# Performance work log

Hardware: AMD Instinct MI355X
Metric: run time of the kernel (lower is better)

## Reference

```python
import jax, jax.numpy as jnp
import numpy as np

NUM_GROUPS = 32
EPS = 1e-6


def group_norm(x, gamma, beta):
    # x: (B, C, H, W)
    B, C, H, W = x.shape
    g = x.reshape(B, NUM_GROUPS, C // NUM_GROUPS, H, W)
    mean = g.mean(axis=(2, 3, 4), keepdims=True)
    var = g.var(axis=(2, 3, 4), keepdims=True)
    g = (g - mean) / jnp.sqrt(var + EPS)
    g = g.reshape(B, C, H, W)
    return g * gamma[None, :, None, None] + beta[None, :, None, None]


def nin(x, W, b):
    # 1x1 linear projection over channel dim
    return jnp.einsum('bchw,cd->bdhw', x, W) + b[None, :, None, None]


def setup_inputs() -> dict:
    key = jax.random.key(0)
    ks = jax.random.split(key, 8)
    B, C, H, W = 32, 512, 32, 32
    lim = np.sqrt(3 * 0.1 / C)  # NIN init_scale=0.1 uniform limit
    return {
        'x': jax.random.normal(ks[0], (B, C, H, W), jnp.float32),
        'gamma': jnp.ones((C,), jnp.float32),
        'beta': jnp.zeros((C,), jnp.float32),
        'Wq': jax.random.uniform(ks[1], (C, C), jnp.float32, -lim, lim),
        'bq': jnp.zeros((C,), jnp.float32),
        'Wk': jax.random.uniform(ks[2], (C, C), jnp.float32, -lim, lim),
        'bk': jnp.zeros((C,), jnp.float32),
        'Wv': jax.random.uniform(ks[3], (C, C), jnp.float32, -lim, lim),
        'bv': jnp.zeros((C,), jnp.float32),
        'Wp': jax.random.normal(ks[4], (C, C), jnp.float32) * 1e-5,  # init_scale=0.0 -> ~0
        'bp': jnp.zeros((C,), jnp.float32),
    }


def reference(x, gamma, beta, Wq, bq, Wk, bk, Wv, bv, Wp, bp):
    B, C, H, W = x.shape
    h = group_norm(x, gamma, beta)
    q = nin(h, Wq, bq)
    k = nin(h, Wk, bk)
    v = nin(h, Wv, bv)
    # full (HW)x(HW) attention weights, as the original materializes
    w = jnp.einsum('bchw,bcHW->bhwHW', q, k) * (C ** -0.5)
    w = w.reshape(B, H, W, H * W)
    w = jax.nn.softmax(w, axis=-1)
    w = w.reshape(B, H, W, H, W)
    h_out = jnp.einsum('bhwHW,bcHW->bchw', w, v)
    h_out = nin(h_out, Wp, bp)
    return x + h_out
```

## Files before the change

kernel.cpp:

```cpp
#include <hip/hip_runtime.h>
#include <hip/hip_bf16.h>
#include <math.h>

typedef __attribute__((ext_vector_type(8))) short bf16x8;
typedef __attribute__((ext_vector_type(4))) float f32x4;

typedef const __attribute__((address_space(1))) unsigned int guint;
typedef __attribute__((address_space(3))) unsigned int luint;

static __device__ __forceinline__ short f2bf(float f) {
    union { float f; unsigned u; } a; a.f = f;
    unsigned r = 0x7FFFu + ((a.u >> 16) & 1u);
    return (short)((a.u + r) >> 16);
}
static __device__ __forceinline__ float bf2f(short s) {
    union { unsigned u; float f; } a;
    a.u = ((unsigned)(unsigned short)s) << 16;
    return a.f;
}

__global__ __launch_bounds__(256)
void transpose_w(const float* __restrict__ w0, const float* __restrict__ w1,
                 const float* __restrict__ w2, const float* __restrict__ w3,
                 short* __restrict__ outT, float qscale)
{
    __shared__ float ld[32][33];
    const float* W = (blockIdx.z == 0) ? w0 : (blockIdx.z == 1) ? w1
                   : (blockIdx.z == 2) ? w2 : w3;
    const float sc = (blockIdx.z == 0) ? qscale : 1.f;
    short* O = outT + (long long)blockIdx.z * 512 * 512;
    const int tx = threadIdx.x & 31, ty = threadIdx.x >> 5;
    const int c0 = blockIdx.y * 32, d0 = blockIdx.x * 32;
#pragma unroll
    for (int r = 0; r < 4; ++r)
        ld[ty + 8 * r][tx] = W[(long long)(c0 + ty + 8 * r) * 512 + d0 + tx];
    __syncthreads();
#pragma unroll
    for (int r = 0; r < 4; ++r)
        O[(long long)(d0 + ty + 8 * r) * 512 + c0 + tx] = f2bf(ld[tx][ty + 8 * r] * sc);
}

__global__ __launch_bounds__(256)
void concat_bias(const float* __restrict__ bq, const float* __restrict__ bk,
                 float* __restrict__ bqk, float qscale)
{
    int i = blockIdx.x * 256 + threadIdx.x;
    bqk[i] = (i < 512) ? bq[i] * qscale : bk[i - 512];
}

__global__ __launch_bounds__(256)
void gn_stats(const float* __restrict__ x, float2* __restrict__ stats)
{
    const int bg = blockIdx.x;
    const float4* p = reinterpret_cast<const float4*>(x + (long long)bg * 16384);
    float s = 0.f, ss = 0.f;
    for (int i = threadIdx.x; i < 4096; i += 256) {
        float4 v = p[i];
        s  += v.x + v.y + v.z + v.w;
        ss += v.x * v.x + v.y * v.y + v.z * v.z + v.w * v.w;
    }
    __shared__ float rs[256], rss[256];
    rs[threadIdx.x] = s; rss[threadIdx.x] = ss;
    __syncthreads();
    for (int o = 128; o > 0; o >>= 1) {
        if (threadIdx.x < o) { rs[threadIdx.x] += rs[threadIdx.x + o];
                               rss[threadIdx.x] += rss[threadIdx.x + o]; }
        __syncthreads();
    }
    if (threadIdx.x == 0) {
        float mean = rs[0] * (1.f / 16384.f);
        float var  = rss[0] * (1.f / 16384.f) - mean * mean;
        stats[bg] = make_float2(mean, rsqrtf(var + 1e-6f));
    }
}

__global__ __launch_bounds__(256)
void gn_apply_t(const float* __restrict__ x, const float2* __restrict__ stats,
                const float* __restrict__ gamma, const float* __restrict__ beta,
                short* __restrict__ hn)
{
    __shared__ short lds[32 * 520];
    const int t = threadIdx.x;
    const int s0 = blockIdx.x * 32;
    const int b  = blockIdx.y;
#pragma unroll
    for (int i = 0; i < 16; ++i) {
        int qi = t + 256 * i;
        int c = qi >> 3, sc = qi & 7;
        float4 v = *reinterpret_cast<const float4*>(
            x + ((long long)(b * 512 + c)) * 1024 + s0 + sc * 4);
        float2 st = stats[b * 32 + (c >> 4)];
        float ga = gamma[c], be = beta[c];
        float m = st.x, r = st.y;
        lds[(sc * 4 + 0) * 520 + c] = f2bf((v.x - m) * r * ga + be);
        lds[(sc * 4 + 1) * 520 + c] = f2bf((v.y - m) * r * ga + be);
        lds[(sc * 4 + 2) * 520 + c] = f2bf((v.z - m) * r * ga + be);
        lds[(sc * 4 + 3) * 520 + c] = f2bf((v.w - m) * r * ga + be);
    }
    __syncthreads();
#pragma unroll
    for (int i = 0; i < 8; ++i) {
        int p = t + 256 * i;
        int s = p >> 6, j = p & 63;
        float4 v = *reinterpret_cast<const float4*>(&lds[s * 520 + j * 8]);
        *reinterpret_cast<float4*>(
            hn + ((long long)(b * 1024 + s0 + s)) * 512 + j * 8) = v;
    }
}

template<int BIAS_M, int BIAS_N, int RESID, int EXPOUT, int DIVROW>
__global__ __launch_bounds__(512, 2)
void nt_gemm(const short* __restrict__ A, const short* __restrict__ B,
             void* __restrict__ Cv,
             const float* __restrict__ biasM, const float* __restrict__ biasN,
             const float* __restrict__ resid, const float* __restrict__ rs,
             int rsM, float scale, int K, int lda, int ldb, int ldc,
             long long sA, long long sB, long long sC,
             int tilesM, int tilesPerBatch)
{
    __shared__ short lsA[2][256 * 64];
    __shared__ short lsB[2][256 * 64];

    const int id = blockIdx.x;
    const int chunk = gridDim.x >> 3;
    const int gid = (id & 7) * chunk + (id >> 3);
    const int bz = gid / tilesPerBatch;
    const int tt = gid - bz * tilesPerBatch;
    const int m0 = (tt % tilesM) * 256;
    const int n0 = (tt / tilesM) * 256;

    const int t = threadIdx.x;
    const int lane = t & 63;
    const int w = t >> 6;
    const int wm = w >> 2, wn = w & 3;
    const int lr16 = lane & 15, lkg = lane >> 4;
    const int sw = lr16 & 7;

    const int srow = t >> 3;
    const int scol = ((t & 7) ^ ((t >> 3) & 7)) * 8;
    const short* gA = A + (long long)bz * sA + (long long)(m0 + srow) * lda + scol;
    const short* gB = B + (long long)bz * sB + (long long)(n0 + srow) * ldb + scol;

    f32x4 acc[8][4];
#pragma unroll
    for (int i = 0; i < 8; ++i)
#pragma unroll
        for (int j = 0; j < 4; ++j) acc[i][j] = (f32x4){0.f, 0.f, 0.f, 0.f};

    const int nk = K >> 6;

#define STAGE(buf, kt)                                                         \
    {                                                                          \
        const short* ga_ = gA + (kt) * 64;                                     \
        const short* gb_ = gB + (kt) * 64;                                     \
        _Pragma("unroll")                                                      \
        for (int c = 0; c < 4; ++c) {                                          \
            __builtin_amdgcn_global_load_lds(                                  \
                (guint*)(ga_ + (long long)(64 * c) * lda),                     \
                (luint*)&lsA[buf][t * 8 + 4096 * c], 16, 0, 0);                \
            __builtin_amdgcn_global_load_lds(                                  \
                (guint*)(gb_ + (long long)(64 * c) * ldb),                     \
                (luint*)&lsB[buf][t * 8 + 4096 * c], 16, 0, 0);                \
        }                                                                      \
    }

#define COMPUTE(buf)                                                           \
    {                                                                          \
        _Pragma("unroll")                                                      \
        for (int ks = 0; ks < 2; ++ks) {                                       \
            bf16x8 bq[4];                                                      \
            _Pragma("unroll")                                                  \
            for (int ni = 0; ni < 4; ++ni)                                     \
                bq[ni] = *reinterpret_cast<const bf16x8*>(                     \
                    &lsB[buf][(wn * 64 + ni * 16 + lr16) * 64 +                \
                              (((ks * 4 + lkg) ^ sw) * 8)]);                   \
            _Pragma("unroll")                                                  \
            for (int mq = 0; mq < 4; ++mq) {                                   \
                bf16x8 aq[2];                                                  \
                _Pragma("unroll")                                              \
                for (int z = 0; z < 2; ++z)                                    \
                    aq[z] = *reinterpret_cast<const bf16x8*>(                  \
                        &lsA[buf][(wm * 128 + (mq * 2 + z) * 16 + lr16) * 64 + \
                                  (((ks * 4 + lkg) ^ sw) * 8)]);               \
                __builtin_amdgcn_s_setprio(1);                                 \
                _Pragma("unroll")                                              \
                for (int z = 0; z < 2; ++z)                                    \
                    _Pragma("unroll")                                          \
                    for (int ni = 0; ni < 4; ++ni)                             \
                        acc[mq * 2 + z][ni] =                                  \
                            __builtin_amdgcn_mfma_f32_16x16x32_bf16(           \
                                aq[z], bq[ni], acc[mq * 2 + z][ni], 0, 0, 0);  \
                __builtin_amdgcn_s_setprio(0);                                 \
            }                                                                  \
        }                                                                      \
    }

    STAGE(0, 0);
    int cur = 0;
    for (int kt = 0; kt < nk - 1; ++kt) {
        STAGE(cur ^ 1, kt + 1);
        asm volatile("s_waitcnt vmcnt(8)" ::: "memory");
        __builtin_amdgcn_sched_barrier(0);
        __builtin_amdgcn_s_barrier();
        __builtin_amdgcn_sched_barrier(0);
        COMPUTE(cur);
        __builtin_amdgcn_sched_barrier(0);
        __builtin_amdgcn_s_barrier();
        __builtin_amdgcn_sched_barrier(0);
        cur ^= 1;
    }
    asm volatile("s_waitcnt vmcnt(0)" ::: "memory");
    __builtin_amdgcn_sched_barrier(0);
    __builtin_amdgcn_s_barrier();
    __builtin_amdgcn_sched_barrier(0);
    COMPUTE(cur);
#undef STAGE
#undef COMPUTE

#pragma unroll
    for (int mi = 0; mi < 8; ++mi) {
        float addm[4], mul[4];
#pragma unroll
        for (int j = 0; j < 4; ++j) {
            const int rrow = m0 + wm * 128 + mi * 16 + lkg * 4 + j;
            addm[j] = BIAS_M ? biasM[rrow] : 0.f;
            mul[j]  = DIVROW ? 1.f / rs[(long long)bz * rsM + rrow] : 1.f;
        }
#pragma unroll
        for (int ni = 0; ni < 4; ++ni) {
            const int col = n0 + wn * 64 + ni * 16 + lr16;
            float bn = BIAS_N ? biasN[col] : 0.f;
#pragma unroll
            for (int j = 0; j < 4; ++j) {
                const int rrow = m0 + wm * 128 + mi * 16 + lkg * 4 + j;
                float v2 = acc[mi][ni][j] + addm[j] + bn;
                v2 *= scale;
                if (EXPOUT) v2 = __expf(v2 - 8.f);
                if (DIVROW) v2 *= mul[j];
                const long long idx = (long long)rrow * ldc + col;
                if (RESID) {
                    float* Cf = (float*)Cv + (long long)bz * sC;
                    Cf[idx] = v2 + resid[(long long)bz * sC + idx];
                } else {
                    short* Cs = (short*)Cv + (long long)bz * sC;
                    Cs[idx] = f2bf(v2);
                }
            }
        }
    }
}

__global__ __launch_bounds__(256)
void rowsum_rows(const short* __restrict__ S, float* __restrict__ rs)
{
    const int wave = threadIdx.x >> 6, lane = threadIdx.x & 63;
    const long long row = (long long)blockIdx.x * 4 + wave;
    const short* p = S + row * 1024;
    bf16x8 h0 = *reinterpret_cast<const bf16x8*>(p + lane * 8);
    bf16x8 h1 = *reinterpret_cast<const bf16x8*>(p + 512 + lane * 8);
    float s = 0.f;
#pragma unroll
    for (int j = 0; j < 8; ++j) s += bf2f(h0[j]) + bf2f(h1[j]);
#pragma unroll
    for (int o = 32; o > 0; o >>= 1) s += __shfl_xor(s, o);
    if (lane == 0) rs[row] = s;
}

extern "C" void kernel_launch(void* const* d_in, const int* in_sizes, int n_in,
                              void* d_out, int out_size, void* d_ws, size_t ws_size,
                              hipStream_t stream)
{
    (void)in_sizes; (void)n_in; (void)out_size; (void)ws_size;
    const float* x     = (const float*)d_in[0];
    const float* gamma = (const float*)d_in[1];
    const float* beta  = (const float*)d_in[2];
    const float* Wq = (const float*)d_in[3];
    const float* bq = (const float*)d_in[4];
    const float* Wk = (const float*)d_in[5];
    const float* bk = (const float*)d_in[6];
    const float* Wv = (const float*)d_in[7];
    const float* bv = (const float*)d_in[8];
    const float* Wp = (const float*)d_in[9];
    const float* bp = (const float*)d_in[10];
    float* out = (float*)d_out;

    char* ws = (char*)d_ws;
    short*  expS = (short*)ws;
    short*  hn   = (short*)ws;
    short*  qkb  = (short*)(ws + (64LL << 20));
    short*  vbuf = (short*)(ws + (128LL << 20));
    short*  wT   = (short*)(ws + (160LL << 20));
    float2* stats = (float2*)(ws + (162LL << 20));
    float*  bqk   = (float*)(ws + (162LL << 20) + (16 << 10));
    float*  rs    = (float*)(ws + (162LL << 20) + (32 << 10));
    short*  ho    = qkb;

    const short* WqkT = wT;
    const short* WvT  = wT + 2 * 512 * 512;
    const short* WpT  = wT + 3 * 512 * 512;

    const float qscale = 0.044194173824159216f;

    transpose_w<<<dim3(16, 16, 4), 256, 0, stream>>>(Wq, Wk, Wv, Wp, wT, qscale);
    concat_bias<<<dim3(4), 256, 0, stream>>>(bq, bk, bqk, qscale);
    gn_stats<<<dim3(1024), 256, 0, stream>>>(x, stats);
    gn_apply_t<<<dim3(32, 32), 256, 0, stream>>>(x, stats, gamma, beta, hn);

    nt_gemm<0, 1, 0, 0, 0><<<512, 512, 0, stream>>>(
        hn, WqkT, qkb, nullptr, bqk, nullptr, nullptr, 0, 1.f,
        512, 512, 512, 1024, 1024 * 512, 0, 1024LL * 1024, 4, 16);
    nt_gemm<1, 0, 0, 0, 0><<<256, 512, 0, stream>>>(
        WvT, hn, vbuf, bv, nullptr, nullptr, nullptr, 0, 1.f,
        512, 512, 512, 1024, 0, 1024 * 512, 512 * 1024, 2, 8);
    nt_gemm<0, 0, 0, 1, 0><<<512, 512, 0, stream>>>(
        qkb, qkb + 512, expS, nullptr, nullptr, nullptr, nullptr, 0, 1.f,
        512, 1024, 1024, 1024, 1024LL * 1024, 1024LL * 1024, 1024LL * 1024, 4, 16);
    rowsum_rows<<<dim3(8192), 256, 0, stream>>>(expS, rs);
    nt_gemm<0, 0, 0, 0, 1><<<256, 512, 0, stream>>>(
        expS, vbuf, ho, nullptr, nullptr, nullptr, rs, 1024, 1.f,
        1024, 1024, 1024, 512, 1024LL * 1024, 512 * 1024, 1024 * 512, 4, 8);
    nt_gemm<1, 0, 1, 0, 0><<<256, 512, 0, stream>>>(
        WpT, ho, out, bp, nullptr, x, nullptr, 0, 1.f,
        512, 512, 512, 1024, 0, 1024 * 512, 512LL * 1024, 2, 8);
}
```

Before: 247.2 us.

## Split GEMM tiles into quadrant phases with interleaved half-tile prefetch

Restructures the 256x256 bf16 NT GEMM main loop into four phases per k-step, each computing one 128x128 quadrant. Each phase issues the global-to-LDS load for one half of the next A or B tile, separated by barriers and explicit vmcnt waits. Wave tiling changes from 2x4 to 4x2, and LDS fragments are loaded once per phase before the MFMA burst. The aim is finer-grained overlap of memory traffic with MFMA work. In exchange it adds more barriers and prefetches past the end of K on the last iterations, which assumes an even tile count and readable memory beyond the final tile.

```diff
diff --git a/kernel.cpp b/kernel.cpp
--- a/kernel.cpp
+++ b/kernel.cpp
@@ -118,8 +118,8 @@
              long long sA, long long sB, long long sC,
              int tilesM, int tilesPerBatch)
 {
-    __shared__ short lsA[2][256 * 64];
-    __shared__ short lsB[2][256 * 64];
+    __shared__ short lsA[2][2][128 * 64];
+    __shared__ short lsB[2][2][128 * 64];
 
     const int id = blockIdx.x;
     const int chunk = gridDim.x >> 3;
@@ -132,118 +132,141 @@
     const int t = threadIdx.x;
     const int lane = t & 63;
     const int w = t >> 6;
-    const int wm = w >> 2, wn = w & 3;
+    const int wrs = w >> 1;
+    const int wcs = w & 1;
     const int lr16 = lane & 15, lkg = lane >> 4;
     const int sw = lr16 & 7;
 
     const int srow = t >> 3;
-    const int scol = ((t & 7) ^ ((t >> 3) & 7)) * 8;
+    const int scol = ((t & 7) ^ (srow & 7)) * 8;
     const short* gA = A + (long long)bz * sA + (long long)(m0 + srow) * lda + scol;
     const short* gB = B + (long long)bz * sB + (long long)(n0 + srow) * ldb + scol;
 
-    f32x4 acc[8][4];
-#pragma unroll
-    for (int i = 0; i < 8; ++i)
-#pragma unroll
-        for (int j = 0; j < 4; ++j) acc[i][j] = (f32x4){0.f, 0.f, 0.f, 0.f};
+    f32x4 acc[4][2][4];
+#pragma unroll
+    for (int q = 0; q < 4; ++q)
+#pragma unroll
+        for (int i = 0; i < 2; ++i)
+#pragma unroll
+            for (int j = 0; j < 4; ++j) acc[q][i][j] = (f32x4){0.f, 0.f, 0.f, 0.f};
 
     const int nk = K >> 6;
 
-#define STAGE(buf, kt)                                                         \
+#define STAGE_A(buf, h, kt)                                                    \
     {                                                                          \
-        const short* ga_ = gA + (kt) * 64;                                     \
-        const short* gb_ = gB + (kt) * 64;                                     \
-        _Pragma("unroll")                                                      \
-        for (int c = 0; c < 4; ++c) {                                          \
+        _Pragma("unroll")                                                      \
+        for (int c = 0; c < 2; ++c)                                            \
             __builtin_amdgcn_global_load_lds(                                  \
-                (guint*)(ga_ + (long long)(64 * c) * lda),                     \
-                (luint*)&lsA[buf][t * 8 + 4096 * c], 16, 0, 0);                \
+                (guint*)(gA + (long long)((h) * 128 + 64 * c) * lda + (kt) * 64), \
+                (luint*)&lsA[buf][h][t * 8 + 4096 * c], 16, 0, 0);             \
+    }
+#define STAGE_B(buf, h, kt)                                                    \
+    {                                                                          \
+        _Pragma("unroll")                                                      \
+        for (int c = 0; c < 2; ++c)                                            \
             __builtin_amdgcn_global_load_lds(                                  \
-                (guint*)(gb_ + (long long)(64 * c) * ldb),                     \
-                (luint*)&lsB[buf][t * 8 + 4096 * c], 16, 0, 0);                \
-        }                                                                      \
-    }
-
-#define COMPUTE(buf)                                                           \
+                (guint*)(gB + (long long)((h) * 128 + 64 * c) * ldb + (kt) * 64), \
+                (luint*)&lsB[buf][h][t * 8 + 4096 * c], 16, 0, 0);             \
+    }
+#define VM6 asm volatile("s_waitcnt vmcnt(6)" ::: "memory")
+#define VM8 asm volatile("s_waitcnt vmcnt(8)" ::: "memory")
+#define NOPV ((void)0)
+
+#define PHASE(buf, ah, bh, SOP, VM)                                            \
     {                                                                          \
-        _Pragma("unroll")                                                      \
-        for (int ks = 0; ks < 2; ++ks) {                                       \
-            bf16x8 bq[4];                                                      \
+        bf16x8 af[2][2], bfr[4][2];                                            \
+        _Pragma("unroll")                                                      \
+        for (int mi2 = 0; mi2 < 2; ++mi2)                                      \
             _Pragma("unroll")                                                  \
-            for (int ni = 0; ni < 4; ++ni)                                     \
-                bq[ni] = *reinterpret_cast<const bf16x8*>(                     \
-                    &lsB[buf][(wn * 64 + ni * 16 + lr16) * 64 +                \
-                              (((ks * 4 + lkg) ^ sw) * 8)]);                   \
+            for (int ks = 0; ks < 2; ++ks)                                     \
+                af[mi2][ks] = *reinterpret_cast<const bf16x8*>(                \
+                    &lsA[buf][ah][(wrs * 32 + mi2 * 16 + lr16) * 64 +          \
+                                  (((ks * 4 + lkg) ^ sw) * 8)]);               \
+        _Pragma("unroll")                                                      \
+        for (int ni = 0; ni < 4; ++ni)                                         \
             _Pragma("unroll")                                                  \
-            for (int mq = 0; mq < 4; ++mq) {                                   \
-                bf16x8 aq[2];                                                  \
+            for (int ks = 0; ks < 2; ++ks)                                     \
+                bfr[ni][ks] = *reinterpret_cast<const bf16x8*>(                \
+                    &lsB[buf][bh][(wcs * 64 + ni * 16 + lr16) * 64 +           \
+                                  (((ks * 4 + lkg) ^ sw) * 8)]);               \
+        SOP;                                                                   \
+        __builtin_amdgcn_s_barrier();                                          \
+        asm volatile("s_waitcnt lgkmcnt(0)" ::: "memory");                     \
+        __builtin_amdgcn_sched_barrier(0);                                     \
+        __builtin_amdgcn_s_setprio(1);                                         \
+        _Pragma("unroll")                                                      \
+        for (int ks = 0; ks < 2; ++ks)                                         \
+            _Pragma("unroll")                                                  \
+            for (int mi2 = 0; mi2 < 2; ++mi2)                                  \
                 _Pragma("unroll")                                              \
-                for (int z = 0; z < 2; ++z)                                    \
-                    aq[z] = *reinterpret_cast<const bf16x8*>(                  \
-                        &lsA[buf][(wm * 128 + (mq * 2 + z) * 16 + lr16) * 64 + \
-                                  (((ks * 4 + lkg) ^ sw) * 8)]);               \
-                __builtin_amdgcn_s_setprio(1);                                 \
-                _Pragma("unroll")                                              \
-                for (int z = 0; z < 2; ++z)                                    \
-                    _Pragma("unroll")                                          \
-                    for (int ni = 0; ni < 4; ++ni)                             \
-                        acc[mq * 2 + z][ni] =                                  \
-                            __builtin_amdgcn_mfma_f32_16x16x32_bf16(           \
-                                aq[z], bq[ni], acc[mq * 2 + z][ni], 0, 0, 0);  \
-                __builtin_amdgcn_s_setprio(0);                                 \
-            }                                                                  \
-        }                                                                      \
-    }
-
-    STAGE(0, 0);
-    int cur = 0;
-    for (int kt = 0; kt < nk - 1; ++kt) {
-        STAGE(cur ^ 1, kt + 1);
-        asm volatile("s_waitcnt vmcnt(8)" ::: "memory");
-        __builtin_amdgcn_sched_barrier(0);
-        __builtin_amdgcn_s_barrier();
-        __builtin_amdgcn_sched_barrier(0);
-        COMPUTE(cur);
-        __builtin_amdgcn_sched_barrier(0);
-        __builtin_amdgcn_s_barrier();
-        __builtin_amdgcn_sched_barrier(0);
-        cur ^= 1;
-    }
-    asm volatile("s_waitcnt vmcnt(0)" ::: "memory");
+                for (int ni = 0; ni < 4; ++ni)                                 \
+                    acc[(ah) * 2 + (bh)][mi2][ni] =                            \
+                        __builtin_amdgcn_mfma_f32_16x16x32_bf16(               \
+                            af[mi2][ks], bfr[ni][ks],                          \
+                            acc[(ah) * 2 + (bh)][mi2][ni], 0, 0, 0);           \
+        __builtin_amdgcn_s_setprio(0);                                         \
+        __builtin_amdgcn_sched_barrier(0);                                     \
+        VM;                                                                    \
+        __builtin_amdgcn_s_barrier();                                          \
+    }
+
+#define FRAME(b, kt)                                                           \
+    PHASE(b, 0, 0, STAGE_A((b) ^ 1, 1, (kt) + 1), VM6)                         \
+    PHASE(b, 0, 1, STAGE_B((b) ^ 1, 1, (kt) + 1), NOPV)                        \
+    PHASE(b, 1, 0, STAGE_A(b, 0, (kt) + 2), NOPV)                              \
+    PHASE(b, 1, 1, STAGE_B(b, 0, (kt) + 2), VM8)
+
+    STAGE_A(0, 0, 0); STAGE_B(0, 0, 0); STAGE_A(0, 1, 0); STAGE_B(0, 1, 0);
+    STAGE_A(1, 0, 1); STAGE_B(1, 0, 1);
+    asm volatile("s_waitcnt vmcnt(4)" ::: "memory");
     __builtin_amdgcn_sched_barrier(0);
     __builtin_amdgcn_s_barrier();
-    __builtin_amdgcn_sched_barrier(0);
-    COMPUTE(cur);
-#undef STAGE
-#undef COMPUTE
-
-#pragma unroll
-    for (int mi = 0; mi < 8; ++mi) {
-        float addm[4], mul[4];
-#pragma unroll
-        for (int j = 0; j < 4; ++j) {
-            const int rrow = m0 + wm * 128 + mi * 16 + lkg * 4 + j;
-            addm[j] = BIAS_M ? biasM[rrow] : 0.f;
-            mul[j]  = DIVROW ? 1.f / rs[(long long)bz * rsM + rrow] : 1.f;
-        }
-#pragma unroll
-        for (int ni = 0; ni < 4; ++ni) {
-            const int col = n0 + wn * 64 + ni * 16 + lr16;
-            float bn = BIAS_N ? biasN[col] : 0.f;
-#pragma unroll
-            for (int j = 0; j < 4; ++j) {
-                const int rrow = m0 + wm * 128 + mi * 16 + lkg * 4 + j;
-                float v2 = acc[mi][ni][j] + addm[j] + bn;
-                v2 *= scale;
-                if (EXPOUT) v2 = __expf(v2 - 8.f);
-                if (DIVROW) v2 *= mul[j];
-                const long long idx = (long long)rrow * ldc + col;
-                if (RESID) {
-                    float* Cf = (float*)Cv + (long long)bz * sC;
-                    Cf[idx] = v2 + resid[(long long)bz * sC + idx];
-                } else {
-                    short* Cs = (short*)Cv + (long long)bz * sC;
-                    Cs[idx] = f2bf(v2);
+
+    for (int kt = 0; kt < nk; kt += 2) {
+        FRAME(0, kt)
+        FRAME(1, kt + 1)
+    }
+#undef STAGE_A
+#undef STAGE_B
+#undef PHASE
+#undef FRAME
+#undef VM6
+#undef VM8
+#undef NOPV
+
+#pragma unroll
+    for (int ah = 0; ah < 2; ++ah) {
+#pragma unroll
+        for (int bh = 0; bh < 2; ++bh) {
+#pragma unroll
+            for (int mi2 = 0; mi2 < 2; ++mi2) {
+                float addm[4], mul[4];
+#pragma unroll
+                for (int j = 0; j < 4; ++j) {
+                    const int rrow = m0 + ah * 128 + wrs * 32 + mi2 * 16 + lkg * 4 + j;
+                    addm[j] = BIAS_M ? biasM[rrow] : 0.f;
+                    mul[j]  = DIVROW ? 1.f / rs[(long long)bz * rsM + rrow] : 1.f;
+                }
+#pragma unroll
+                for (int ni = 0; ni < 4; ++ni) {
+                    const int col = n0 + bh * 128 + wcs * 64 + ni * 16 + lr16;
+                    float bn = BIAS_N ? biasN[col] : 0.f;
+#pragma unroll
+                    for (int j = 0; j < 4; ++j) {
+                        const int rrow = m0 + ah * 128 + wrs * 32 + mi2 * 16 + lkg * 4 + j;
+                        float v2 = acc[ah * 2 + bh][mi2][ni][j] + addm[j] + bn;
+                        v2 *= scale;
+                        if (EXPOUT) v2 = __expf(v2 - 8.f);
+                        if (DIVROW) v2 *= mul[j];
+                        const long long idx = (long long)rrow * ldc + col;
+                        if (RESID) {
+                            float* Cf = (float*)Cv + (long long)bz * sC;
+                            Cf[idx] = v2 + resid[(long long)bz * sC + idx];
+                        } else {
+                            short* Cs = (short*)Cv + (long long)bz * sC;
+                            Cs[idx] = f2bf(v2);
+                        }
+                    }
                 }
             }
         }
```

Measured after the change: 255.9 us. 3.5% more time.
